# Kernel optimization log

Hardware: AMD Instinct MI355X
Metric: run time of the kernel (lower is better)

The kernel has to match this reference:

```python
import jax, jax.numpy as jnp
import numpy as np

B, W, C, N = 16, 512, 4096, 8  # batch, words, coordinates, heads; k = C//N == W required by module math


def setup_inputs() -> dict:
    key = jax.random.key(0)
    ks = jax.random.split(key, 6)
    return {
        "x": jax.random.normal(ks[0], (B, W, C), dtype=jnp.float32),
        "W1": jax.random.normal(ks[1], (C, C), dtype=jnp.float32) * 0.02,
        "b1": jax.random.normal(ks[2], (C,), dtype=jnp.float32) * 0.02,
        "pre_metric": jax.random.normal(ks[3], (N, W, W), dtype=jnp.float32) * 0.02,
        "W2": jax.random.normal(ks[4], (C, C), dtype=jnp.float32) * 0.02,
        "b2": jax.random.normal(ks[5], (C,), dtype=jnp.float32) * 0.02,
    }


def reference(x, W1, b1, pre_metric, W2, b2):
    b, w, c = x.shape
    n = pre_metric.shape[0]
    k = c // n  # == w by construction
    tril = jnp.tril(jnp.ones((w, w), dtype=x.dtype))
    # causal-masked lower-triangular factor, metric M = L L^T per head
    L = pre_metric * tril                         # (n, w, w)
    M = jnp.einsum('nuv,nwv->nuw', L, L)          # (n, w, w)
    # single shared projection
    P = (x @ W1.T + b1).reshape(b, w, n, k).transpose(0, 2, 1, 3)  # (b, n, w, k)
    # bilinear quadratic form scores: P^T M P  -> (b, n, k, k) with k == w
    MP = jnp.einsum('nuv,bnvj->bnuj', M, P)       # (b, n, w, k)
    S = jnp.einsum('bnui,bnuj->bnij', P, MP)      # (b, n, k, k)
    S = S / jnp.sqrt(jnp.asarray(k, x.dtype))
    # causal zero-fill (no softmax)
    S = S * tril
    out = jnp.einsum('bnij,bnjk->bnik', S, P)     # (b, n, w, k)
    out = out.transpose(0, 2, 1, 3).reshape(b, w, c)
    return out @ W2.T + b2
```

## Files before the change

kernel.cpp:

```cpp
#include <hip/hip_runtime.h>
#include <stdint.h>

typedef uint16_t u16;
typedef short short8 __attribute__((ext_vector_type(8)));
typedef float f32x4 __attribute__((ext_vector_type(4)));

__device__ __forceinline__ u16 f2bf(float f){
  uint32_t u = __float_as_uint(f);
  u += 0x7fff + ((u >> 16) & 1);
  return (u16)(u >> 16);
}

__device__ __forceinline__ void gload_lds16(const u16* g, const char* l){
  __builtin_amdgcn_global_load_lds((const __attribute__((address_space(1))) void*)g,
                                   (__attribute__((address_space(3))) void*)l,
                                   16, 0, 0);
}

__global__ void cast_bf16_kernel(const float* __restrict__ src, u16* __restrict__ dst, long n8){
  long i = (long)blockIdx.x * blockDim.x + threadIdx.x;
  long stride = (long)gridDim.x * blockDim.x;
  for (; i < n8; i += stride){
    float4 a = *(const float4*)(src + i*8);
    float4 b = *(const float4*)(src + i*8 + 4);
    u16 r[8] = {f2bf(a.x), f2bf(a.y), f2bf(a.z), f2bf(a.w),
                f2bf(b.x), f2bf(b.y), f2bf(b.z), f2bf(b.w)};
    *(uint4*)(dst + i*8) = *(const uint4*)r;
  }
}

__global__ void mask_cast_L_kernel(const float* __restrict__ pre, u16* __restrict__ L){
  long i = (long)blockIdx.x * blockDim.x + threadIdx.x;
  if (i >= 8L*512*64) return;
  int v0 = (int)(i & 63) * 8;
  int u  = (int)((i >> 6) & 511);
  float4 a = *(const float4*)(pre + i*8);
  float4 b = *(const float4*)(pre + i*8 + 4);
  float vals[8] = {a.x,a.y,a.z,a.w,b.x,b.y,b.z,b.w};
  u16 r[8];
  #pragma unroll
  for (int j=0;j<8;j++) r[j] = f2bf((v0 + j <= u) ? vals[j] : 0.0f);
  *(uint4*)(L + i*8) = *(const uint4*)r;
}

template<int EPI>
__global__ __launch_bounds__(512, 1)
void gemm_nt2(const u16* __restrict__ A, const u16* __restrict__ B,
              void* __restrict__ Cv, int K, int lda, int ldb, int ldc,
              long asb, long asn, long bsb, long bsn, long csb, long csn,
              const float* __restrict__ bias, float scale, int tri)
{
  extern __shared__ __align__(16) char smem[];
  const int t = threadIdx.x;
  const int lane = t & 63;
  const int wave = t >> 6;
  const int wm = wave >> 2;
  const int wn = wave & 3;
  const long zb = blockIdx.z >> 3, zn = blockIdx.z & 7;
  A += zb*asb + zn*asn;
  B += zb*bsb + zn*bsn;
  const int row0 = blockIdx.y * 256, col0 = blockIdx.x * 256;

  if (tri == 1 && col0 >= row0 + 256) return;

  const int l15 = lane & 15, l4 = lane >> 4;

  const int srow = t >> 2;
  const int scol = (((t & 3) ^ ((srow >> 1) & 3)) * 8);
  const u16* gA = A + (long)(row0 + srow)*lda + scol;
  const u16* gB = B + (long)(col0 + srow)*ldb + scol;
  const long a128 = 128L*(long)lda, b128 = 128L*(long)ldb;
  const int ldst = t * 16;

  const int csw = (l4 ^ ((l15 >> 1) & 3)) * 16;
  const int raw = (wm*128 + l15)*64 + csw;
  const int rbw = 16384 + (wn*64 + l15)*64 + csw;

  f32x4 acc[8][4];
  #pragma unroll
  for (int m=0;m<8;m++)
    #pragma unroll
    for (int n=0;n<4;n++) acc[m][n] = (f32x4){0.f,0.f,0.f,0.f};

  int Keff = K;
  if (tri == 2) Keff = (row0 + 256 < K) ? (row0 + 256) : K;
  const int NT = Keff >> 5;

#define STG_A(PA, BUF) \
  gload_lds16((PA),        smem + (BUF)*32768 +         ldst); \
  gload_lds16((PA) + a128, smem + (BUF)*32768 +  8192 + ldst);
#define STG_B(PB, BUF) \
  gload_lds16((PB),        smem + (BUF)*32768 + 16384 + ldst); \
  gload_lds16((PB) + b128, smem + (BUF)*32768 + 24576 + ldst);

#define WAITB(VM) \
  asm volatile("s_waitcnt vmcnt(" VM ")" ::: "memory"); \
  __builtin_amdgcn_s_barrier(); \
  asm volatile("" ::: "memory");

#define COMPUTE(BUF, S1, S2) { \
  const char* base = smem + (BUF)*32768; \
  short8 bfr[4], afr[4]; \
  _Pragma("unroll") \
  for (int n=0;n<4;n++) bfr[n] = *(const short8*)(base + rbw + n*1024); \
  _Pragma("unroll") \
  for (int m=0;m<4;m++) afr[m] = *(const short8*)(base + raw + m*1024); \
  S1 \
  __builtin_amdgcn_s_setprio(1); \
  _Pragma("unroll") \
  for (int m=0;m<4;m++) \
    _Pragma("unroll") \
    for (int n=0;n<4;n++) \
      acc[m][n] = __builtin_amdgcn_mfma_f32_16x16x32_bf16(afr[m], bfr[n], acc[m][n],0,0,0); \
  __builtin_amdgcn_s_setprio(0); \
  _Pragma("unroll") \
  for (int m=0;m<4;m++) afr[m] = *(const short8*)(base + raw + (m+4)*1024); \
  S2 \
  __builtin_amdgcn_s_setprio(1); \
  _Pragma("unroll") \
  for (int m=0;m<4;m++) \
    _Pragma("unroll") \
    for (int n=0;n<4;n++) \
      acc[m+4][n] = __builtin_amdgcn_mfma_f32_16x16x32_bf16(afr[m], bfr[n], acc[m+4][n],0,0,0); \
  __builtin_amdgcn_s_setprio(0); \
}

  STG_A(gA,      0) STG_B(gB,      0)
  STG_A(gA + 32, 1) STG_B(gB + 32, 1)
  STG_A(gA + 64, 2) STG_B(gB + 64, 2)

  #pragma unroll 1
  for (int tb = 0; tb < NT - 4; tb += 4){
    const u16* pa = gA + (long)(tb + 3)*32;
    const u16* pb = gB + (long)(tb + 3)*32;
    WAITB("8"); COMPUTE(0, STG_A(pa,      3), STG_B(pb,      3));
    WAITB("8"); COMPUTE(1, STG_A(pa + 32, 0), STG_B(pb + 32, 0));
    WAITB("8"); COMPUTE(2, STG_A(pa + 64, 1), STG_B(pb + 64, 1));
    WAITB("8"); COMPUTE(3, STG_A(pa + 96, 2), STG_B(pb + 96, 2));
  }
  {
    const u16* pa = gA + (long)(NT - 1)*32;
    const u16* pb = gB + (long)(NT - 1)*32;
    WAITB("8"); COMPUTE(0, STG_A(pa, 3), STG_B(pb, 3));
    WAITB("8"); COMPUTE(1, , );
    WAITB("4"); COMPUTE(2, , );
    WAITB("0"); COMPUTE(3, , );
  }
#undef STG_A
#undef STG_B
#undef WAITB
#undef COMPUTE

  if constexpr (EPI == 3){
    float* C = (float*)Cv;
    #pragma unroll
    for (int m=0;m<8;m++){
      int r0 = row0 + wm*128 + m*16 + l4*4;
      #pragma unroll
      for (int n=0;n<4;n++){
        int c = col0 + wn*64 + n*16 + l15;
        float bc = bias[c];
        #pragma unroll
        for (int g=0; g<4; g++)
          C[(long)(r0+g)*ldc + c] = acc[m][n][g] + bc;
      }
    }
  } else {
    u16* C = (u16*)Cv + zb*csb + zn*csn;
    #pragma unroll
    for (int m=0;m<8;m++){
      int r0 = row0 + wm*128 + m*16 + l4*4;
      #pragma unroll
      for (int n=0;n<4;n++){
        int c = col0 + wn*64 + n*16 + l15;
        #pragma unroll
        for (int g=0;g<4;g++){
          float v = acc[m][n][g];
          int r = r0 + g;
          if constexpr (EPI==1) v += bias[r];
          if constexpr (EPI==2) v = (c <= r) ? v*scale : 0.0f;
          C[(long)r*ldc + c] = f2bf(v);
        }
      }
    }
  }
}


#define LDSB 131072

extern "C" void kernel_launch(void* const* d_in, const int* in_sizes, int n_in,
                              void* d_out, int out_size, void* d_ws, size_t ws_size,
                              hipStream_t stream)
{
  (void)in_sizes; (void)n_in; (void)out_size; (void)ws_size;
  const float* x   = (const float*)d_in[0];
  const float* W1  = (const float*)d_in[1];
  const float* b1  = (const float*)d_in[2];
  const float* pre = (const float*)d_in[3];
  const float* W2  = (const float*)d_in[4];
  const float* b2  = (const float*)d_in[5];
  float* out = (float*)d_out;
  char* ws = (char*)d_ws;

  u16* xb  = (u16*)(ws + 0L);
  u16* W1b = (u16*)(ws + 67108864L);
  u16* W2b = (u16*)(ws + 100663296L);
  u16* Lb  = (u16*)(ws + 134217728L);
  u16* Mb  = (u16*)(ws + 138412032L);
  u16* Pt  = (u16*)(ws + 142606336L);
  u16* MPt = (u16*)(ws + 209715200L);
  u16* Sb  = (u16*)(ws + 276824064L);
  u16* Ob  = MPt;

  hipFuncSetAttribute((const void*)gemm_nt2<0>, hipFuncAttributeMaxDynamicSharedMemorySize, LDSB);
  hipFuncSetAttribute((const void*)gemm_nt2<1>, hipFuncAttributeMaxDynamicSharedMemorySize, LDSB);
  hipFuncSetAttribute((const void*)gemm_nt2<2>, hipFuncAttributeMaxDynamicSharedMemorySize, LDSB);
  hipFuncSetAttribute((const void*)gemm_nt2<3>, hipFuncAttributeMaxDynamicSharedMemorySize, LDSB);

  cast_bf16_kernel<<<4096,256,0,stream>>>(x,  xb,  4194304L);
  cast_bf16_kernel<<<4096,256,0,stream>>>(W1, W1b, 2097152L);
  cast_bf16_kernel<<<4096,256,0,stream>>>(W2, W2b, 2097152L);
  mask_cast_L_kernel<<<1024,256,0,stream>>>(pre, Lb);

  gemm_nt2<0><<<dim3(2,2,8),512,LDSB,stream>>>(Lb, Lb, Mb, 512, 512,512,512,
      0, 262144, 0, 262144, 0, 262144, nullptr, 0.f, 0);

  gemm_nt2<1><<<dim3(32,16,1),512,LDSB,stream>>>(W1b, xb, Pt, 4096, 4096,4096,8192,
      0,0, 0,0, 0,0, b1, 0.f, 0);

  gemm_nt2<0><<<dim3(2,2,128),512,LDSB,stream>>>(Pt, Mb, MPt, 512, 8192,512,512,
      512, 512L*8192, 0, 262144, 8L*262144, 262144, nullptr, 0.f, 0);

  gemm_nt2<2><<<dim3(2,2,128),512,LDSB,stream>>>(Pt, MPt, Sb, 512, 8192,512,512,
      512, 512L*8192, 8L*262144, 262144, 8L*262144, 262144, nullptr, 0.04419417382f, 1);

  gemm_nt2<0><<<dim3(2,2,128),512,LDSB,stream>>>(Sb, Pt, Ob, 512, 512,8192,4096,
      8L*262144, 262144, 512, 512L*8192, 512L*4096, 512, nullptr, 0.f, 2);

  gemm_nt2<3><<<dim3(16,32,1),512,LDSB,stream>>>(Ob, W2b, out, 4096, 4096,4096,4096,
      0,0, 0,0, 0,0, b2, 0.f, 0);
}
```

Baseline: 703.1 us.

## Double-buffer LDS fragment reads in GEMM and merge three cast kernels

Reworks the GEMM main loop so the LDS-to-register fragments for the next K-step are loaded into a second register set while MFMAs run on the current one. This hides LDS read latency behind matrix math and puts the barrier after compute. It also fuses the three fp32-to-bf16 cast launches into one kernel to cut launch overhead. The cost is roughly double the fragment registers and a more delicate vmcnt and barrier schedule across the four-deep LDS ring.

```diff
diff --git a/kernel.cpp b/kernel.cpp
--- a/kernel.cpp
+++ b/kernel.cpp
@@ -17,15 +17,21 @@
                                    16, 0, 0);
 }
 
-__global__ void cast_bf16_kernel(const float* __restrict__ src, u16* __restrict__ dst, long n8){
+__global__ void cast3_kernel(const float* __restrict__ x, const float* __restrict__ W1,
+                             const float* __restrict__ W2, u16* __restrict__ xb,
+                             u16* __restrict__ W1b, u16* __restrict__ W2b){
   long i = (long)blockIdx.x * blockDim.x + threadIdx.x;
   long stride = (long)gridDim.x * blockDim.x;
-  for (; i < n8; i += stride){
-    float4 a = *(const float4*)(src + i*8);
-    float4 b = *(const float4*)(src + i*8 + 4);
+  for (; i < 8388608L; i += stride){
+    const float* s; u16* d; long off;
+    if (i < 4194304L){ s = x;  d = xb;  off = i; }
+    else if (i < 6291456L){ s = W1; d = W1b; off = i - 4194304L; }
+    else { s = W2; d = W2b; off = i - 6291456L; }
+    float4 a = *(const float4*)(s + off*8);
+    float4 b = *(const float4*)(s + off*8 + 4);
     u16 r[8] = {f2bf(a.x), f2bf(a.y), f2bf(a.z), f2bf(a.w),
                 f2bf(b.x), f2bf(b.y), f2bf(b.z), f2bf(b.w)};
-    *(uint4*)(dst + i*8) = *(const uint4*)r;
+    *(uint4*)(d + off*8) = *(const uint4*)r;
   }
 }
 
@@ -45,7 +51,7 @@
 
 template<int EPI>
 __global__ __launch_bounds__(512, 1)
-void gemm_nt2(const u16* __restrict__ A, const u16* __restrict__ B,
+void gemm_nt3(const u16* __restrict__ A, const u16* __restrict__ B,
               void* __restrict__ Cv, int K, int lda, int ldb, int ldc,
               long asb, long asn, long bsb, long bsn, long csb, long csn,
               const float* __restrict__ bias, float scale, int tri)
@@ -86,70 +92,72 @@
   if (tri == 2) Keff = (row0 + 256 < K) ? (row0 + 256) : K;
   const int NT = Keff >> 5;
 
-#define STG_A(PA, BUF) \
+  short8 afr[2][8], bfr[2][4];
+
+#define STG(PA, PB, BUF) \
   gload_lds16((PA),        smem + (BUF)*32768 +         ldst); \
-  gload_lds16((PA) + a128, smem + (BUF)*32768 +  8192 + ldst);
-#define STG_B(PB, BUF) \
+  gload_lds16((PA) + a128, smem + (BUF)*32768 +  8192 + ldst); \
   gload_lds16((PB),        smem + (BUF)*32768 + 16384 + ldst); \
   gload_lds16((PB) + b128, smem + (BUF)*32768 + 24576 + ldst);
 
-#define WAITB(VM) \
-  asm volatile("s_waitcnt vmcnt(" VM ")" ::: "memory"); \
+#define RDS(S, BUF) { \
+  const char* b_ = smem + (BUF)*32768; \
+  _Pragma("unroll") \
+  for (int n=0;n<4;n++) bfr[S][n] = *(const short8*)(b_ + rbw + n*1024); \
+  _Pragma("unroll") \
+  for (int m=0;m<8;m++) afr[S][m] = *(const short8*)(b_ + raw + m*1024); }
+
+#define MM(S) { \
+  __builtin_amdgcn_s_setprio(1); \
+  _Pragma("unroll") \
+  for (int m=0;m<8;m++) \
+    _Pragma("unroll") \
+    for (int n=0;n<4;n++) \
+      acc[m][n] = __builtin_amdgcn_mfma_f32_16x16x32_bf16(afr[S][m], bfr[S][n], acc[m][n],0,0,0); \
+  __builtin_amdgcn_s_setprio(0); }
+
+#define ENDB(VMS) \
+  asm volatile("s_waitcnt vmcnt(" VMS ")" ::: "memory"); \
   __builtin_amdgcn_s_barrier(); \
   asm volatile("" ::: "memory");
 
-#define COMPUTE(BUF, S1, S2) { \
-  const char* base = smem + (BUF)*32768; \
-  short8 bfr[4], afr[4]; \
-  _Pragma("unroll") \
-  for (int n=0;n<4;n++) bfr[n] = *(const short8*)(base + rbw + n*1024); \
-  _Pragma("unroll") \
-  for (int m=0;m<4;m++) afr[m] = *(const short8*)(base + raw + m*1024); \
-  S1 \
-  __builtin_amdgcn_s_setprio(1); \
-  _Pragma("unroll") \
-  for (int m=0;m<4;m++) \
-    _Pragma("unroll") \
-    for (int n=0;n<4;n++) \
-      acc[m][n] = __builtin_amdgcn_mfma_f32_16x16x32_bf16(afr[m], bfr[n], acc[m][n],0,0,0); \
-  __builtin_amdgcn_s_setprio(0); \
-  _Pragma("unroll") \
-  for (int m=0;m<4;m++) afr[m] = *(const short8*)(base + raw + (m+4)*1024); \
-  S2 \
-  __builtin_amdgcn_s_setprio(1); \
-  _Pragma("unroll") \
-  for (int m=0;m<4;m++) \
-    _Pragma("unroll") \
-    for (int n=0;n<4;n++) \
-      acc[m+4][n] = __builtin_amdgcn_mfma_f32_16x16x32_bf16(afr[m], bfr[n], acc[m+4][n],0,0,0); \
-  __builtin_amdgcn_s_setprio(0); \
-}
-
-  STG_A(gA,      0) STG_B(gB,      0)
-  STG_A(gA + 32, 1) STG_B(gB + 32, 1)
-  STG_A(gA + 64, 2) STG_B(gB + 64, 2)
+#define BODY(P, Q, NXT, DOST, PA, PB, VMS) { \
+  RDS(Q, NXT) \
+  if (DOST){ STG(PA, PB, ((NXT)+2)&3) } \
+  __builtin_amdgcn_sched_barrier(0); \
+  MM(P) \
+  ENDB(VMS) }
+
+  STG(gA,      gB,      0)
+  STG(gA + 32, gB + 32, 1)
+  STG(gA + 64, gB + 64, 2)
+  asm volatile("s_waitcnt vmcnt(4)" ::: "memory");
+  __builtin_amdgcn_s_barrier();
+  asm volatile("" ::: "memory");
+  RDS(0, 0)
 
   #pragma unroll 1
   for (int tb = 0; tb < NT - 4; tb += 4){
     const u16* pa = gA + (long)(tb + 3)*32;
     const u16* pb = gB + (long)(tb + 3)*32;
-    WAITB("8"); COMPUTE(0, STG_A(pa,      3), STG_B(pb,      3));
-    WAITB("8"); COMPUTE(1, STG_A(pa + 32, 0), STG_B(pb + 32, 0));
-    WAITB("8"); COMPUTE(2, STG_A(pa + 64, 1), STG_B(pb + 64, 1));
-    WAITB("8"); COMPUTE(3, STG_A(pa + 96, 2), STG_B(pb + 96, 2));
+    BODY(0, 1, 1, true, pa,      pb,      "4")
+    BODY(1, 0, 2, true, pa + 32, pb + 32, "4")
+    BODY(0, 1, 3, true, pa + 64, pb + 64, "4")
+    BODY(1, 0, 0, true, pa + 96, pb + 96, "4")
   }
   {
     const u16* pa = gA + (long)(NT - 1)*32;
     const u16* pb = gB + (long)(NT - 1)*32;
-    WAITB("8"); COMPUTE(0, STG_A(pa, 3), STG_B(pb, 3));
-    WAITB("8"); COMPUTE(1, , );
-    WAITB("4"); COMPUTE(2, , );
-    WAITB("0"); COMPUTE(3, , );
-  }
-#undef STG_A
-#undef STG_B
-#undef WAITB
-#undef COMPUTE
+    BODY(0, 1, 1, true,  pa, pb, "4")
+    BODY(1, 0, 2, false, pa, pb, "0")
+    BODY(0, 1, 3, false, pa, pb, "0")
+    MM(1)
+  }
+#undef STG
+#undef RDS
+#undef MM
+#undef ENDB
+#undef BODY
 
   if constexpr (EPI == 3){
     float* C = (float*)Cv;
@@ -213,31 +221,29 @@
   u16* Sb  = (u16*)(ws + 276824064L);
   u16* Ob  = MPt;
 
-  hipFuncSetAttribute((const void*)gemm_nt2<0>, hipFuncAttributeMaxDynamicSharedMemorySize, LDSB);
-  hipFuncSetAttribute((const void*)gemm_nt2<1>, hipFuncAttributeMaxDynamicSharedMemorySize, LDSB);
-  hipFuncSetAttribute((const void*)gemm_nt2<2>, hipFuncAttributeMaxDynamicSharedMemorySize, LDSB);
-  hipFuncSetAttribute((const void*)gemm_nt2<3>, hipFuncAttributeMaxDynamicSharedMemorySize, LDSB);
-
-  cast_bf16_kernel<<<4096,256,0,stream>>>(x,  xb,  4194304L);
-  cast_bf16_kernel<<<4096,256,0,stream>>>(W1, W1b, 2097152L);
-  cast_bf16_kernel<<<4096,256,0,stream>>>(W2, W2b, 2097152L);
+  hipFuncSetAttribute((const void*)gemm_nt3<0>, hipFuncAttributeMaxDynamicSharedMemorySize, LDSB);
+  hipFuncSetAttribute((const void*)gemm_nt3<1>, hipFuncAttributeMaxDynamicSharedMemorySize, LDSB);
+  hipFuncSetAttribute((const void*)gemm_nt3<2>, hipFuncAttributeMaxDynamicSharedMemorySize, LDSB);
+  hipFuncSetAttribute((const void*)gemm_nt3<3>, hipFuncAttributeMaxDynamicSharedMemorySize, LDSB);
+
+  cast3_kernel<<<4096,256,0,stream>>>(x, W1, W2, xb, W1b, W2b);
   mask_cast_L_kernel<<<1024,256,0,stream>>>(pre, Lb);
 
-  gemm_nt2<0><<<dim3(2,2,8),512,LDSB,stream>>>(Lb, Lb, Mb, 512, 512,512,512,
+  gemm_nt3<0><<<dim3(2,2,8),512,LDSB,stream>>>(Lb, Lb, Mb, 512, 512,512,512,
       0, 262144, 0, 262144, 0, 262144, nullptr, 0.f, 0);
 
-  gemm_nt2<1><<<dim3(32,16,1),512,LDSB,stream>>>(W1b, xb, Pt, 4096, 4096,4096,8192,
+  gemm_nt3<1><<<dim3(32,16,1),512,LDSB,stream>>>(W1b, xb, Pt, 4096, 4096,4096,8192,
       0,0, 0,0, 0,0, b1, 0.f, 0);
 
-  gemm_nt2<0><<<dim3(2,2,128),512,LDSB,stream>>>(Pt, Mb, MPt, 512, 8192,512,512,
+  gemm_nt3<0><<<dim3(2,2,128),512,LDSB,stream>>>(Pt, Mb, MPt, 512, 8192,512,512,
       512, 512L*8192, 0, 262144, 8L*262144, 262144, nullptr, 0.f, 0);
 
-  gemm_nt2<2><<<dim3(2,2,128),512,LDSB,stream>>>(Pt, MPt, Sb, 512, 8192,512,512,
+  gemm_nt3<2><<<dim3(2,2,128),512,LDSB,stream>>>(Pt, MPt, Sb, 512, 8192,512,512,
       512, 512L*8192, 8L*262144, 262144, 8L*262144, 262144, nullptr, 0.04419417382f, 1);
 
-  gemm_nt2<0><<<dim3(2,2,128),512,LDSB,stream>>>(Sb, Pt, Ob, 512, 512,8192,4096,
+  gemm_nt3<0><<<dim3(2,2,128),512,LDSB,stream>>>(Sb, Pt, Ob, 512, 512,8192,4096,
       8L*262144, 262144, 512, 512L*8192, 512L*4096, 512, nullptr, 0.f, 2);
 
-  gemm_nt2<3><<<dim3(16,32,1),512,LDSB,stream>>>(Ob, W2b, out, 4096, 4096,4096,4096,
+  gemm_nt3<3><<<dim3(16,32,1),512,LDSB,stream>>>(Ob, W2b, out, 4096, 4096,4096,4096,
       0,0, 0,0, 0,0, b2, 0.f, 0);
 }
```

Result: slower. 945.8 us (+34.5%).
